# Kernel optimization log

Measured on AMD Instinct MI355X. Metric: run time of the kernel, lower is better.

Reference implementation:

```python
import jax, jax.numpy as jnp
import numpy as np

EPS = 1e-8

def setup_inputs() -> dict:
    key = jax.random.key(0)
    k1, k2, k3, k4, k5 = jax.random.split(key, 5)
    B, S, d, H = 4, 1024, 512, 8
    hd = d // H
    x = jax.random.normal(k1, (B, S, d), dtype=jnp.float32)
    V = jax.random.normal(k2, (B, S, H, hd), dtype=jnp.float32)
    # binary biological mask [B, S, S]
    M = (jax.random.uniform(k3, (B, S, S)) > 0.5).astype(jnp.float32)
    in_proj_w = jax.random.normal(k4, (3 * d, d), dtype=jnp.float32) * 0.02
    in_proj_b = jnp.zeros((3 * d,), dtype=jnp.float32)
    out_w = jax.random.normal(k5, (d, d), dtype=jnp.float32) * 0.02
    out_b = jnp.zeros((d,), dtype=jnp.float32)
    return {"x": x, "V": V, "M": M, "in_proj_w": in_proj_w,
            "in_proj_b": in_proj_b, "out_w": out_w, "out_b": out_b}


def reference(x, V, M, in_proj_w, in_proj_b, out_w, out_b):
    B, S, d = x.shape
    H, hd = V.shape[2], V.shape[3]
    # packed QKV projection (torch MHA in_proj); V slice is computed by torch
    # but its result is discarded, so only Q,K slices influence the output.
    qkv = x @ in_proj_w.T + in_proj_b            # [B, S, 3d]
    q = qkv[..., :d].reshape(B, S, H, hd).transpose(0, 2, 1, 3)        # [B,H,S,hd]
    k = qkv[..., d:2 * d].reshape(B, S, H, hd).transpose(0, 2, 1, 3)   # [B,H,S,hd]
    scores = jnp.einsum("bhqd,bhkd->bhqk", q, k) / jnp.sqrt(jnp.float32(hd))
    A = jax.nn.softmax(scores, axis=-1)           # [B,H,S,S] per-head attn weights
    # biological mask + L1 renormalization (post-hoc, as in original)
    A_sparse = A * M[:, None, :, :]
    norm = jnp.sum(jnp.abs(A_sparse), axis=-1, keepdims=True) + EPS
    A_bar = A_sparse / norm
    # custom V: [B,S,H,hd] -> [B,H,S,hd]
    Vp = V.transpose(0, 2, 1, 3)
    out = jnp.einsum("bhqk,bhkd->bhqd", A_bar, Vp)  # [B,H,S,hd]
    out = out.transpose(0, 2, 1, 3).reshape(B, S, d)
    return out @ out_w.T + out_b
```

## Files before the change

### kernel.cpp

```cpp
#include <hip/hip_runtime.h>
#include <hip/hip_bf16.h>

#define BB 4
#define SS 1024
#define DD 512
#define HH 8
#define HD 64

typedef __attribute__((ext_vector_type(8))) short bf16x8;
typedef __attribute__((ext_vector_type(4))) float f32x4;

static __device__ __forceinline__ unsigned short f2b(float f) {
  union { float f; unsigned int u; } c; c.f = f;
  return (unsigned short)((c.u + 0x7fffu + ((c.u >> 16) & 1u)) >> 16);
}

__global__ __launch_bounds__(256) void prep(
    const float* __restrict__ x, const float* __restrict__ W1,
    const float* __restrict__ Wo, const float* __restrict__ Mmask,
    const float* __restrict__ V, unsigned short* __restrict__ xb,
    unsigned short* __restrict__ W1b, unsigned short* __restrict__ Wob,
    unsigned char* __restrict__ Mpack, unsigned short* __restrict__ Vt) {
  __shared__ float Ls[64][65];
  const int bid = blockIdx.x;
  const int tid = threadIdx.x;

  if (bid < 1408) {
    const float* src; unsigned short* dst; size_t off;
    if (bid < 1024) { src = x;  dst = xb;  off = ((size_t)bid * 256 + tid) * 8; }
    else if (bid < 1280) { src = W1; dst = W1b; off = ((size_t)(bid - 1024) * 256 + tid) * 8; }
    else { src = Wo; dst = Wob; off = ((size_t)(bid - 1280) * 256 + tid) * 8; }
    const float4 a = *(const float4*)(src + off);
    const float4 b = *(const float4*)(src + off + 4);
    union { unsigned short s[8]; uint4 v; } o;
    o.s[0] = f2b(a.x); o.s[1] = f2b(a.y); o.s[2] = f2b(a.z); o.s[3] = f2b(a.w);
    o.s[4] = f2b(b.x); o.s[5] = f2b(b.y); o.s[6] = f2b(b.z); o.s[7] = f2b(b.w);
    *(uint4*)(dst + off) = o.v;
  } else if (bid < 3456) {
    const size_t g = (size_t)(bid - 1408) * 256 + tid;
    const float4 a = *(const float4*)(Mmask + g * 8);
    const float4 b = *(const float4*)(Mmask + g * 8 + 4);
    unsigned v = 0;
    v |= (a.x > 0.5f) ? 1u : 0u;   v |= (a.y > 0.5f) ? 2u : 0u;
    v |= (a.z > 0.5f) ? 4u : 0u;   v |= (a.w > 0.5f) ? 8u : 0u;
    v |= (b.x > 0.5f) ? 16u : 0u;  v |= (b.y > 0.5f) ? 32u : 0u;
    v |= (b.z > 0.5f) ? 64u : 0u;  v |= (b.w > 0.5f) ? 128u : 0u;
    Mpack[g] = (unsigned char)v;
  } else {
    const int id = bid - 3456;
    const int s0 = (id & 15) * 64, h = (id >> 4) & 7, b = id >> 7;
    {
      const int r = tid >> 2, cs = (tid & 3) * 16;
      const float* src = V + ((size_t)((b * SS + s0 + r) * HH) + h) * HD + cs;
#pragma unroll
      for (int j = 0; j < 4; j++) {
        const float4 v = *(const float4*)(src + j * 4);
        Ls[r][cs + j * 4 + 0] = v.x; Ls[r][cs + j * 4 + 1] = v.y;
        Ls[r][cs + j * 4 + 2] = v.z; Ls[r][cs + j * 4 + 3] = v.w;
      }
    }
    __syncthreads();
    {
      const int d = tid >> 2, ss = (tid & 3) * 16;
      union { unsigned short s[16]; uint4 v[2]; } o;
#pragma unroll
      for (int j = 0; j < 16; j++) o.s[j] = f2b(Ls[ss + j][d]);
      unsigned short* dst =
          Vt + ((size_t)((b * HH + h) * HD + d)) * SS + s0 + ss;
      *(uint4*)dst = o.v[0];
      *(uint4*)(dst + 8) = o.v[1];
    }
  }
}

__global__ __launch_bounds__(256) void gemm_qk(
    const unsigned short* __restrict__ xb, const unsigned short* __restrict__ W1b,
    const float* __restrict__ bias, unsigned short* __restrict__ qkb) {
  __shared__ unsigned short As[128][40];
  __shared__ unsigned short Bs[64][40];
  const int tid = threadIdx.x;
  const int lane = tid & 63, wave = tid >> 6;
  const int l16 = lane & 15, quad = lane >> 4;
  const int row0 = blockIdx.y * 128, col0 = blockIdx.x * 64;

  f32x4 acc[2][4];
#pragma unroll
  for (int i = 0; i < 2; i++)
#pragma unroll
    for (int j = 0; j < 4; j++) acc[i][j] = (f32x4){0.f, 0.f, 0.f, 0.f};

  const int ra = tid >> 1, csa = (tid & 1) * 16;
  const int rb = tid >> 2, csb = (tid & 3) * 8;
  const unsigned short* ap = xb + (size_t)(row0 + ra) * DD + csa;
  const unsigned short* bp = W1b + (size_t)(col0 + rb) * DD + csb;

  uint4 pa0 = *(const uint4*)ap, pa1 = *(const uint4*)(ap + 8);
  uint4 pb = *(const uint4*)bp;

  for (int k0 = 0; k0 < DD; k0 += 32) {
    __syncthreads();
    *(uint4*)&As[ra][csa] = pa0;
    *(uint4*)&As[ra][csa + 8] = pa1;
    *(uint4*)&Bs[rb][csb] = pb;
    __syncthreads();
    if (k0 + 32 < DD) {
      pa0 = *(const uint4*)(ap + k0 + 32);
      pa1 = *(const uint4*)(ap + k0 + 40);
      pb = *(const uint4*)(bp + k0 + 32);
    }

    const bf16x8 a0 = *(const bf16x8*)&As[wave * 32 + l16][quad * 8];
    const bf16x8 a1 = *(const bf16x8*)&As[wave * 32 + 16 + l16][quad * 8];
#pragma unroll
    for (int nt = 0; nt < 4; nt++) {
      const bf16x8 bb = *(const bf16x8*)&Bs[nt * 16 + l16][quad * 8];
      acc[0][nt] = __builtin_amdgcn_mfma_f32_16x16x32_bf16(a0, bb, acc[0][nt], 0, 0, 0);
      acc[1][nt] = __builtin_amdgcn_mfma_f32_16x16x32_bf16(a1, bb, acc[1][nt], 0, 0, 0);
    }
  }

#pragma unroll
  for (int nt = 0; nt < 4; nt++) {
    const int col = col0 + nt * 16 + l16;
    const float bv = bias[col];
    const float scale = (col < DD) ? 0.125f : 1.0f;
#pragma unroll
    for (int mi = 0; mi < 2; mi++)
#pragma unroll
      for (int reg = 0; reg < 4; reg++) {
        const int row = row0 + wave * 32 + mi * 16 + quad * 4 + reg;
        qkb[(size_t)row * 1024 + col] = f2b((acc[mi][nt][reg] + bv) * scale);
      }
  }
}

__global__ __launch_bounds__(256) void gemm_out(
    const unsigned short* __restrict__ Ab, const unsigned short* __restrict__ Wob,
    const float* __restrict__ bias, float* __restrict__ out) {
  __shared__ unsigned short As[64][40];
  __shared__ unsigned short Bs[64][40];
  const int tid = threadIdx.x;
  const int lane = tid & 63, wave = tid >> 6;
  const int l16 = lane & 15, quad = lane >> 4;
  const int row0 = blockIdx.y * 64, col0 = blockIdx.x * 64;

  f32x4 acc[4];
#pragma unroll
  for (int j = 0; j < 4; j++) acc[j] = (f32x4){0.f, 0.f, 0.f, 0.f};

  const int r = tid >> 2, cs = (tid & 3) * 8;
  const unsigned short* ap = Ab + (size_t)(row0 + r) * DD + cs;
  const unsigned short* bp = Wob + (size_t)(col0 + r) * DD + cs;

  uint4 pa = *(const uint4*)ap;
  uint4 pb = *(const uint4*)bp;

  for (int k0 = 0; k0 < DD; k0 += 32) {
    __syncthreads();
    *(uint4*)&As[r][cs] = pa;
    *(uint4*)&Bs[r][cs] = pb;
    __syncthreads();
    if (k0 + 32 < DD) {
      pa = *(const uint4*)(ap + k0 + 32);
      pb = *(const uint4*)(bp + k0 + 32);
    }

    const bf16x8 a0 = *(const bf16x8*)&As[wave * 16 + l16][quad * 8];
#pragma unroll
    for (int nt = 0; nt < 4; nt++) {
      const bf16x8 bb = *(const bf16x8*)&Bs[nt * 16 + l16][quad * 8];
      acc[nt] = __builtin_amdgcn_mfma_f32_16x16x32_bf16(a0, bb, acc[nt], 0, 0, 0);
    }
  }

#pragma unroll
  for (int nt = 0; nt < 4; nt++) {
    const int col = col0 + nt * 16 + l16;
    const float bv = bias[col];
#pragma unroll
    for (int reg = 0; reg < 4; reg++) {
      const int row = row0 + wave * 16 + quad * 4 + reg;
      out[(size_t)row * DD + col] = acc[nt][reg] + bv;
    }
  }
}

__global__ __launch_bounds__(256) void flash_attn_fused(
    const unsigned short* __restrict__ qkb, const unsigned short* __restrict__ Vt,
    const unsigned char* __restrict__ Mpack, unsigned short* __restrict__ attnb) {
  __shared__ unsigned short Ks[2][64][72];
  __shared__ unsigned short Vs[2][64][72];
  __shared__ unsigned short Pbuf[128][72];
  __shared__ float SmS[2][64];

  const int tid = threadIdx.x;
  const int lane = tid & 63, wave = tid >> 6;
  const int l16 = lane & 15, quad = lane >> 4;
  const int wg = wave & 1, sp = wave >> 1;
  const int q0 = blockIdx.x * 64;
  const int h = blockIdx.y;
  const int b = blockIdx.z;

  const unsigned short* qp =
      qkb + (size_t)(b * SS + q0 + wg * 32 + l16) * 1024 + h * HD + quad * 8;
  const bf16x8 bQa0 = *(const bf16x8*)qp;
  const bf16x8 bQa1 = *(const bf16x8*)(qp + 32);
  const bf16x8 bQb0 = *(const bf16x8*)(qp + 16 * 1024);
  const bf16x8 bQb1 = *(const bf16x8*)(qp + 16 * 1024 + 32);

  const unsigned char* mpa =
      Mpack + (size_t)(b * SS + q0 + wg * 32 + l16) * 128 + sp * 64;
  const unsigned char* mpb = mpa + 16 * 128;
  uint2 pma = *(const uint2*)mpa;
  uint2 pmb = *(const uint2*)mpb;

  const int r = tid >> 2, cs = (tid & 3) * 16;
  const unsigned short* kp0 =
      qkb + (size_t)(b * SS + r) * 1024 + DD + h * HD + cs;
  const unsigned short* kp1 = kp0 + (size_t)512 * 1024;
  const unsigned short* vp0 =
      Vt + ((size_t)((b * HH + h) * HD + r)) * SS + cs;
  const unsigned short* vp1 = vp0 + 512;

  uint4 pk0a = *(const uint4*)kp0, pk0b = *(const uint4*)(kp0 + 8);
  uint4 pk1a = *(const uint4*)kp1, pk1b = *(const uint4*)(kp1 + 8);
  uint4 pv0a = *(const uint4*)vp0, pv0b = *(const uint4*)(vp0 + 8);
  uint4 pv1a = *(const uint4*)vp1, pv1b = *(const uint4*)(vp1 + 8);

  unsigned short(*Ps)[72] = (unsigned short(*)[72]) & Pbuf[wave * 32][0];

  float Sma = 0.f, Smb = 0.f;
  f32x4 Oa[4], Ob[4];
#pragma unroll
  for (int i = 0; i < 4; i++) {
    Oa[i] = (f32x4){0.f, 0.f, 0.f, 0.f};
    Ob[i] = (f32x4){0.f, 0.f, 0.f, 0.f};
  }

  for (int i = 0; i < 8; i++) {
    __syncthreads();
    *(uint4*)&Ks[0][r][cs] = pk0a;
    *(uint4*)&Ks[0][r][cs + 8] = pk0b;
    *(uint4*)&Ks[1][r][cs] = pk1a;
    *(uint4*)&Ks[1][r][cs + 8] = pk1b;
    *(uint4*)&Vs[0][r][cs] = pv0a;
    *(uint4*)&Vs[0][r][cs + 8] = pv0b;
    *(uint4*)&Vs[1][r][cs] = pv1a;
    *(uint4*)&Vs[1][r][cs + 8] = pv1b;
    __syncthreads();

    const uint2 ma = pma, mb = pmb;
    if (i < 7) {
      const size_t ko = (size_t)(i + 1) * 64 * 1024;
      pk0a = *(const uint4*)(kp0 + ko);
      pk0b = *(const uint4*)(kp0 + ko + 8);
      pk1a = *(const uint4*)(kp1 + ko);
      pk1b = *(const uint4*)(kp1 + ko + 8);
      pv0a = *(const uint4*)(vp0 + (i + 1) * 64);
      pv0b = *(const uint4*)(vp0 + (i + 1) * 64 + 8);
      pv1a = *(const uint4*)(vp1 + (i + 1) * 64);
      pv1b = *(const uint4*)(vp1 + (i + 1) * 64 + 8);
      pma = *(const uint2*)(mpa + (i + 1) * 8);
      pmb = *(const uint2*)(mpb + (i + 1) * 8);
    }

#pragma unroll
    for (int t = 0; t < 4; t++) {
      const bf16x8 aK0 = *(const bf16x8*)&Ks[sp][t * 16 + l16][quad * 8];
      const bf16x8 aK1 = *(const bf16x8*)&Ks[sp][t * 16 + l16][32 + quad * 8];
      f32x4 a = (f32x4){0.f, 0.f, 0.f, 0.f};
      a = __builtin_amdgcn_mfma_f32_16x16x32_bf16(aK0, bQa0, a, 0, 0, 0);
      a = __builtin_amdgcn_mfma_f32_16x16x32_bf16(aK1, bQa1, a, 0, 0, 0);
      f32x4 c = (f32x4){0.f, 0.f, 0.f, 0.f};
      c = __builtin_amdgcn_mfma_f32_16x16x32_bf16(aK0, bQb0, c, 0, 0, 0);
      c = __builtin_amdgcn_mfma_f32_16x16x32_bf16(aK1, bQb1, c, 0, 0, 0);

      const unsigned sh = (t & 1) * 16 + quad * 4;
      const unsigned niba = ((t < 2 ? ma.x : ma.y) >> sh) & 0xFu;
      const unsigned nibb = ((t < 2 ? mb.x : mb.y) >> sh) & 0xFu;
      float e0 = __expf(a[0]); e0 = (niba & 1u) ? e0 : 0.f;
      float e1 = __expf(a[1]); e1 = (niba & 2u) ? e1 : 0.f;
      float e2 = __expf(a[2]); e2 = (niba & 4u) ? e2 : 0.f;
      float e3 = __expf(a[3]); e3 = (niba & 8u) ? e3 : 0.f;
      Sma += (e0 + e1) + (e2 + e3);
      uint2 wa;
      wa.x = (unsigned)f2b(e0) | ((unsigned)f2b(e1) << 16);
      wa.y = (unsigned)f2b(e2) | ((unsigned)f2b(e3) << 16);
      *(uint2*)&Ps[l16][t * 16 + quad * 4] = wa;

      float g0 = __expf(c[0]); g0 = (nibb & 1u) ? g0 : 0.f;
      float g1 = __expf(c[1]); g1 = (nibb & 2u) ? g1 : 0.f;
      float g2 = __expf(c[2]); g2 = (nibb & 4u) ? g2 : 0.f;
      float g3 = __expf(c[3]); g3 = (nibb & 8u) ? g3 : 0.f;
      Smb += (g0 + g1) + (g2 + g3);
      uint2 wb;
      wb.x = (unsigned)f2b(g0) | ((unsigned)f2b(g1) << 16);
      wb.y = (unsigned)f2b(g2) | ((unsigned)f2b(g3) << 16);
      *(uint2*)&Ps[16 + l16][t * 16 + quad * 4] = wb;
    }

    const bf16x8 aPa0 = *(const bf16x8*)&Ps[l16][quad * 8];
    const bf16x8 aPa1 = *(const bf16x8*)&Ps[l16][32 + quad * 8];
    const bf16x8 aPb0 = *(const bf16x8*)&Ps[16 + l16][quad * 8];
    const bf16x8 aPb1 = *(const bf16x8*)&Ps[16 + l16][32 + quad * 8];
#pragma unroll
    for (int dt = 0; dt < 4; dt++) {
      const bf16x8 bV0 = *(const bf16x8*)&Vs[sp][dt * 16 + l16][quad * 8];
      const bf16x8 bV1 = *(const bf16x8*)&Vs[sp][dt * 16 + l16][32 + quad * 8];
      Oa[dt] = __builtin_amdgcn_mfma_f32_16x16x32_bf16(aPa0, bV0, Oa[dt], 0, 0, 0);
      Oa[dt] = __builtin_amdgcn_mfma_f32_16x16x32_bf16(aPa1, bV1, Oa[dt], 0, 0, 0);
      Ob[dt] = __builtin_amdgcn_mfma_f32_16x16x32_bf16(aPb0, bV0, Ob[dt], 0, 0, 0);
      Ob[dt] = __builtin_amdgcn_mfma_f32_16x16x32_bf16(aPb1, bV1, Ob[dt], 0, 0, 0);
    }
  }

  Sma += __shfl_xor(Sma, 16);
  Sma += __shfl_xor(Sma, 32);
  Smb += __shfl_xor(Smb, 16);
  Smb += __shfl_xor(Smb, 32);
  if (lane < 16) {
    SmS[sp][wg * 32 + lane] = Sma;
    SmS[sp][wg * 32 + 16 + lane] = Smb;
  }

  __syncthreads();
  float* Of = reinterpret_cast<float*>(&Pbuf[0][0]);
  if (sp == 1) {
#pragma unroll
    for (int dt = 0; dt < 4; dt++)
#pragma unroll
      for (int reg = 0; reg < 4; reg++) {
        const int qa = wg * 32 + quad * 4 + reg;
        Of[qa * 64 + dt * 16 + l16] = Oa[dt][reg];
        Of[(qa + 16) * 64 + dt * 16 + l16] = Ob[dt][reg];
      }
  }
  __syncthreads();

  if (sp == 0) {
#pragma unroll
    for (int dt = 0; dt < 4; dt++)
#pragma unroll
      for (int reg = 0; reg < 4; reg++) {
        const int qa = wg * 32 + quad * 4 + reg;
        const float inva = 1.0f / (SmS[0][qa] + SmS[1][qa] + 1e-12f);
        const float invb = 1.0f / (SmS[0][qa + 16] + SmS[1][qa + 16] + 1e-12f);
        const float va = (Oa[dt][reg] + Of[qa * 64 + dt * 16 + l16]) * inva;
        const float vb = (Ob[dt][reg] + Of[(qa + 16) * 64 + dt * 16 + l16]) * invb;
        attnb[(size_t)(b * SS + q0 + qa) * DD + h * HD + dt * 16 + l16] = f2b(va);
        attnb[(size_t)(b * SS + q0 + qa + 16) * DD + h * HD + dt * 16 + l16] = f2b(vb);
      }
  }
}

extern "C" void kernel_launch(void* const* d_in, const int* in_sizes, int n_in,
                              void* d_out, int out_size, void* d_ws,
                              size_t ws_size, hipStream_t stream) {
  const float* x = (const float*)d_in[0];
  const float* V = (const float*)d_in[1];
  const float* Mmask = (const float*)d_in[2];
  const float* in_proj_w = (const float*)d_in[3];
  const float* in_proj_b = (const float*)d_in[4];
  const float* out_w = (const float*)d_in[5];
  const float* out_b = (const float*)d_in[6];
  float* out = (float*)d_out;

  unsigned char* ws = (unsigned char*)d_ws;
  unsigned short* qkb   = (unsigned short*)(ws);
  unsigned short* xb    = (unsigned short*)(ws + (8ull << 20));
  unsigned short* W1b   = (unsigned short*)(ws + (12ull << 20));
  unsigned short* Wob   = (unsigned short*)(ws + (13ull << 20));
  unsigned short* Vt    = (unsigned short*)(ws + (14ull << 20));
  unsigned short* attnb = (unsigned short*)(ws + (18ull << 20));
  unsigned char*  Mpack = ws + (38ull << 20) + (256u << 10);

  prep<<<3968, 256, 0, stream>>>(x, in_proj_w, out_w, Mmask, V,
                                 xb, W1b, Wob, Mpack, Vt);
  gemm_qk<<<dim3(16, 32), 256, 0, stream>>>(xb, W1b, in_proj_b, qkb);
  flash_attn_fused<<<dim3(SS / 64, HH, BB), 256, 0, stream>>>(
      qkb, Vt, Mpack, attnb);
  gemm_out<<<dim3(8, 64), 256, 0, stream>>>(attnb, Wob, out_b, out);
}
```

Measured before the change: 138.8 us.

## Use 32x32x16 MFMA in attention and pass P via cross-lane shuffles

```diff
diff --git a/kernel.cpp b/kernel.cpp
--- a/kernel.cpp
+++ b/kernel.cpp
@@ -9,6 +9,7 @@
 
 typedef __attribute__((ext_vector_type(8))) short bf16x8;
 typedef __attribute__((ext_vector_type(4))) float f32x4;
+typedef __attribute__((ext_vector_type(16))) float f32x16;
 
 static __device__ __forceinline__ unsigned short f2b(float f) {
   union { float f; unsigned int u; } c; c.f = f;
@@ -190,29 +191,27 @@
     const unsigned char* __restrict__ Mpack, unsigned short* __restrict__ attnb) {
   __shared__ unsigned short Ks[2][64][72];
   __shared__ unsigned short Vs[2][64][72];
-  __shared__ unsigned short Pbuf[128][72];
   __shared__ float SmS[2][64];
+  __shared__ float invS[64];
 
   const int tid = threadIdx.x;
   const int lane = tid & 63, wave = tid >> 6;
-  const int l16 = lane & 15, quad = lane >> 4;
-  const int wg = wave & 1, sp = wave >> 1;
+  const int q31 = lane & 31, hi = lane >> 5;
+  const int qb = (wave & 1) * 32, kh = wave >> 1;
   const int q0 = blockIdx.x * 64;
   const int h = blockIdx.y;
   const int b = blockIdx.z;
 
   const unsigned short* qp =
-      qkb + (size_t)(b * SS + q0 + wg * 32 + l16) * 1024 + h * HD + quad * 8;
-  const bf16x8 bQa0 = *(const bf16x8*)qp;
-  const bf16x8 bQa1 = *(const bf16x8*)(qp + 32);
-  const bf16x8 bQb0 = *(const bf16x8*)(qp + 16 * 1024);
-  const bf16x8 bQb1 = *(const bf16x8*)(qp + 16 * 1024 + 32);
-
-  const unsigned char* mpa =
-      Mpack + (size_t)(b * SS + q0 + wg * 32 + l16) * 128 + sp * 64;
-  const unsigned char* mpb = mpa + 16 * 128;
-  uint2 pma = *(const uint2*)mpa;
-  uint2 pmb = *(const uint2*)mpb;
+      qkb + (size_t)(b * SS + q0 + qb + q31) * 1024 + h * HD;
+  bf16x8 bQ[4];
+#pragma unroll
+  for (int kc = 0; kc < 4; kc++)
+    bQ[kc] = *(const bf16x8*)(qp + kc * 16 + hi * 8);
+
+  const unsigned char* mp =
+      Mpack + (size_t)(b * SS + q0 + qb + q31) * 128 + kh * 64;
+  uint2 pm = *(const uint2*)mp;
 
   const int r = tid >> 2, cs = (tid & 3) * 16;
   const unsigned short* kp0 =
@@ -227,15 +226,12 @@
   uint4 pv0a = *(const uint4*)vp0, pv0b = *(const uint4*)(vp0 + 8);
   uint4 pv1a = *(const uint4*)vp1, pv1b = *(const uint4*)(vp1 + 8);
 
-  unsigned short(*Ps)[72] = (unsigned short(*)[72]) & Pbuf[wave * 32][0];
-
-  float Sma = 0.f, Smb = 0.f;
-  f32x4 Oa[4], Ob[4];
-#pragma unroll
-  for (int i = 0; i < 4; i++) {
-    Oa[i] = (f32x4){0.f, 0.f, 0.f, 0.f};
-    Ob[i] = (f32x4){0.f, 0.f, 0.f, 0.f};
-  }
+  float Smp = 0.f;
+  f32x16 O[2];
+#pragma unroll
+  for (int ds = 0; ds < 2; ds++)
+#pragma unroll
+    for (int j = 0; j < 16; j++) O[ds][j] = 0.f;
 
   for (int i = 0; i < 8; i++) {
     __syncthreads();
@@ -249,7 +245,7 @@
     *(uint4*)&Vs[1][r][cs + 8] = pv1b;
     __syncthreads();
 
-    const uint2 ma = pma, mb = pmb;
+    const uint2 pm_cur = pm;
     if (i < 7) {
       const size_t ko = (size_t)(i + 1) * 64 * 1024;
       pk0a = *(const uint4*)(kp0 + ko);
@@ -260,95 +256,98 @@
       pv0b = *(const uint4*)(vp0 + (i + 1) * 64 + 8);
       pv1a = *(const uint4*)(vp1 + (i + 1) * 64);
       pv1b = *(const uint4*)(vp1 + (i + 1) * 64 + 8);
-      pma = *(const uint2*)(mpa + (i + 1) * 8);
-      pmb = *(const uint2*)(mpb + (i + 1) * 8);
-    }
-
-#pragma unroll
-    for (int t = 0; t < 4; t++) {
-      const bf16x8 aK0 = *(const bf16x8*)&Ks[sp][t * 16 + l16][quad * 8];
-      const bf16x8 aK1 = *(const bf16x8*)&Ks[sp][t * 16 + l16][32 + quad * 8];
-      f32x4 a = (f32x4){0.f, 0.f, 0.f, 0.f};
-      a = __builtin_amdgcn_mfma_f32_16x16x32_bf16(aK0, bQa0, a, 0, 0, 0);
-      a = __builtin_amdgcn_mfma_f32_16x16x32_bf16(aK1, bQa1, a, 0, 0, 0);
-      f32x4 c = (f32x4){0.f, 0.f, 0.f, 0.f};
-      c = __builtin_amdgcn_mfma_f32_16x16x32_bf16(aK0, bQb0, c, 0, 0, 0);
-      c = __builtin_amdgcn_mfma_f32_16x16x32_bf16(aK1, bQb1, c, 0, 0, 0);
-
-      const unsigned sh = (t & 1) * 16 + quad * 4;
-      const unsigned niba = ((t < 2 ? ma.x : ma.y) >> sh) & 0xFu;
-      const unsigned nibb = ((t < 2 ? mb.x : mb.y) >> sh) & 0xFu;
-      float e0 = __expf(a[0]); e0 = (niba & 1u) ? e0 : 0.f;
-      float e1 = __expf(a[1]); e1 = (niba & 2u) ? e1 : 0.f;
-      float e2 = __expf(a[2]); e2 = (niba & 4u) ? e2 : 0.f;
-      float e3 = __expf(a[3]); e3 = (niba & 8u) ? e3 : 0.f;
-      Sma += (e0 + e1) + (e2 + e3);
-      uint2 wa;
-      wa.x = (unsigned)f2b(e0) | ((unsigned)f2b(e1) << 16);
-      wa.y = (unsigned)f2b(e2) | ((unsigned)f2b(e3) << 16);
-      *(uint2*)&Ps[l16][t * 16 + quad * 4] = wa;
-
-      float g0 = __expf(c[0]); g0 = (nibb & 1u) ? g0 : 0.f;
-      float g1 = __expf(c[1]); g1 = (nibb & 2u) ? g1 : 0.f;
-      float g2 = __expf(c[2]); g2 = (nibb & 4u) ? g2 : 0.f;
-      float g3 = __expf(c[3]); g3 = (nibb & 8u) ? g3 : 0.f;
-      Smb += (g0 + g1) + (g2 + g3);
-      uint2 wb;
-      wb.x = (unsigned)f2b(g0) | ((unsigned)f2b(g1) << 16);
-      wb.y = (unsigned)f2b(g2) | ((unsigned)f2b(g3) << 16);
-      *(uint2*)&Ps[16 + l16][t * 16 + quad * 4] = wb;
-    }
-
-    const bf16x8 aPa0 = *(const bf16x8*)&Ps[l16][quad * 8];
-    const bf16x8 aPa1 = *(const bf16x8*)&Ps[l16][32 + quad * 8];
-    const bf16x8 aPb0 = *(const bf16x8*)&Ps[16 + l16][quad * 8];
-    const bf16x8 aPb1 = *(const bf16x8*)&Ps[16 + l16][32 + quad * 8];
-#pragma unroll
-    for (int dt = 0; dt < 4; dt++) {
-      const bf16x8 bV0 = *(const bf16x8*)&Vs[sp][dt * 16 + l16][quad * 8];
-      const bf16x8 bV1 = *(const bf16x8*)&Vs[sp][dt * 16 + l16][32 + quad * 8];
-      Oa[dt] = __builtin_amdgcn_mfma_f32_16x16x32_bf16(aPa0, bV0, Oa[dt], 0, 0, 0);
-      Oa[dt] = __builtin_amdgcn_mfma_f32_16x16x32_bf16(aPa1, bV1, Oa[dt], 0, 0, 0);
-      Ob[dt] = __builtin_amdgcn_mfma_f32_16x16x32_bf16(aPb0, bV0, Ob[dt], 0, 0, 0);
-      Ob[dt] = __builtin_amdgcn_mfma_f32_16x16x32_bf16(aPb1, bV1, Ob[dt], 0, 0, 0);
-    }
-  }
-
-  Sma += __shfl_xor(Sma, 16);
-  Sma += __shfl_xor(Sma, 32);
-  Smb += __shfl_xor(Smb, 16);
-  Smb += __shfl_xor(Smb, 32);
-  if (lane < 16) {
-    SmS[sp][wg * 32 + lane] = Sma;
-    SmS[sp][wg * 32 + 16 + lane] = Smb;
-  }
+      pm = *(const uint2*)(mp + (i + 1) * 8);
+    }
+
+    unsigned Wf[16];
+#pragma unroll
+    for (int ssub = 0; ssub < 2; ssub++) {
+      f32x16 acc;
+#pragma unroll
+      for (int j = 0; j < 16; j++) acc[j] = 0.f;
+#pragma unroll
+      for (int kc = 0; kc < 4; kc++) {
+        const bf16x8 aK =
+            *(const bf16x8*)&Ks[kh][ssub * 32 + q31][kc * 16 + hi * 8];
+        acc = __builtin_amdgcn_mfma_f32_32x32x16_bf16(aK, bQ[kc], acc, 0, 0, 0);
+      }
+      const unsigned msh = (ssub ? pm_cur.y : pm_cur.x) >> (hi * 4);
+#pragma unroll
+      for (int j = 0; j < 4; j++) {
+        float e[4];
+#pragma unroll
+        for (int rr = 0; rr < 4; rr++) {
+          const float ev = __expf(acc[j * 4 + rr]);
+          e[rr] = ((msh >> (8 * j + rr)) & 1u) ? ev : 0.f;
+          Smp += e[rr];
+        }
+        Wf[ssub * 8 + j * 2 + 0] =
+            (unsigned)f2b(e[0]) | ((unsigned)f2b(e[1]) << 16);
+        Wf[ssub * 8 + j * 2 + 1] =
+            (unsigned)f2b(e[2]) | ((unsigned)f2b(e[3]) << 16);
+      }
+    }
+
+    unsigned Rf[8];
+#pragma unroll
+    for (int ssub = 0; ssub < 2; ssub++)
+#pragma unroll
+      for (int kb = 0; kb < 2; kb++)
+#pragma unroll
+        for (int h2 = 0; h2 < 2; h2++) {
+          const unsigned send = hi ? Wf[ssub * 8 + (2 * kb) * 2 + h2]
+                                   : Wf[ssub * 8 + (2 * kb + 1) * 2 + h2];
+          Rf[ssub * 4 + kb * 2 + h2] =
+              (unsigned)__shfl_xor((int)send, 32);
+        }
+
+#pragma unroll
+    for (int ks = 0; ks < 4; ks++) {
+      const int ssub = ks >> 1, kb = ks & 1;
+      union { unsigned u[4]; bf16x8 v; } ap;
+      ap.u[0] = hi ? Rf[ssub * 4 + kb * 2 + 0] : Wf[ssub * 8 + 4 * kb + 0];
+      ap.u[1] = hi ? Rf[ssub * 4 + kb * 2 + 1] : Wf[ssub * 8 + 4 * kb + 1];
+      ap.u[2] = hi ? Wf[ssub * 8 + (2 * kb + 1) * 2 + 0]
+                   : Rf[ssub * 4 + kb * 2 + 0];
+      ap.u[3] = hi ? Wf[ssub * 8 + (2 * kb + 1) * 2 + 1]
+                   : Rf[ssub * 4 + kb * 2 + 1];
+#pragma unroll
+      for (int dsub = 0; dsub < 2; dsub++) {
+        const bf16x8 bV =
+            *(const bf16x8*)&Vs[kh][dsub * 32 + q31][ks * 16 + hi * 8];
+        O[dsub] =
+            __builtin_amdgcn_mfma_f32_32x32x16_bf16(ap.v, bV, O[dsub], 0, 0, 0);
+      }
+    }
+  }
+
+  Smp += __shfl_xor(Smp, 32);
+  if (lane < 32) SmS[kh][qb + lane] = Smp;
 
   __syncthreads();
-  float* Of = reinterpret_cast<float*>(&Pbuf[0][0]);
-  if (sp == 1) {
-#pragma unroll
-    for (int dt = 0; dt < 4; dt++)
-#pragma unroll
-      for (int reg = 0; reg < 4; reg++) {
-        const int qa = wg * 32 + quad * 4 + reg;
-        Of[qa * 64 + dt * 16 + l16] = Oa[dt][reg];
-        Of[(qa + 16) * 64 + dt * 16 + l16] = Ob[dt][reg];
-      }
-  }
+  float* Of = reinterpret_cast<float*>(&Ks[0][0][0]);
+  if (kh == 1) {
+#pragma unroll
+    for (int dsub = 0; dsub < 2; dsub++)
+#pragma unroll
+      for (int reg = 0; reg < 16; reg++) {
+        const int q = qb + (reg & 3) + 8 * (reg >> 2) + 4 * hi;
+        Of[q * 64 + dsub * 32 + q31] = O[dsub][reg];
+      }
+  }
+  if (tid < 64) invS[tid] = 1.0f / (SmS[0][tid] + SmS[1][tid] + 1e-12f);
   __syncthreads();
 
-  if (sp == 0) {
-#pragma unroll
-    for (int dt = 0; dt < 4; dt++)
-#pragma unroll
-      for (int reg = 0; reg < 4; reg++) {
-        const int qa = wg * 32 + quad * 4 + reg;
-        const float inva = 1.0f / (SmS[0][qa] + SmS[1][qa] + 1e-12f);
-        const float invb = 1.0f / (SmS[0][qa + 16] + SmS[1][qa + 16] + 1e-12f);
-        const float va = (Oa[dt][reg] + Of[qa * 64 + dt * 16 + l16]) * inva;
-        const float vb = (Ob[dt][reg] + Of[(qa + 16) * 64 + dt * 16 + l16]) * invb;
-        attnb[(size_t)(b * SS + q0 + qa) * DD + h * HD + dt * 16 + l16] = f2b(va);
-        attnb[(size_t)(b * SS + q0 + qa + 16) * DD + h * HD + dt * 16 + l16] = f2b(vb);
+  if (kh == 0) {
+#pragma unroll
+    for (int dsub = 0; dsub < 2; dsub++)
+#pragma unroll
+      for (int reg = 0; reg < 16; reg++) {
+        const int q = qb + (reg & 3) + 8 * (reg >> 2) + 4 * hi;
+        const float v =
+            (O[dsub][reg] + Of[q * 64 + dsub * 32 + q31]) * invS[q];
+        attnb[(size_t)(b * SS + q0 + q) * DD + h * HD + dsub * 32 + q31] =
+            f2b(v);
       }
   }
 }
```

New measurement: 155.8 us. 1.12x slower.
